# Kernel tuning notes

Hardware: AMD Instinct MI355X
Metric: run time of the kernel (lower is better)

The kernel has to match this reference:

```python
import jax, jax.numpy as jnp
import numpy as np

EPS = 1e-5

def layernorm(x, g, b):
    mu = jnp.mean(x, axis=-1, keepdims=True)
    var = jnp.mean(jnp.square(x - mu), axis=-1, keepdims=True)
    return (x - mu) * jax.lax.rsqrt(var + EPS) * g + b

def rope(x):
    # x: [B, H, S, hd]; faithful to source: theta = 10000**(-2*pos/hd), pos in {0,2,4,...}
    S, hd = x.shape[-2], x.shape[-1]
    pos2 = jnp.arange(0, hd, 2, dtype=jnp.float32)
    theta = jnp.power(10000.0, -2.0 * pos2 / hd)          # [hd/2]
    ang = jnp.arange(S, dtype=jnp.float32)[:, None] * theta  # [S, hd/2]
    cos, sin = jnp.cos(ang), jnp.sin(ang)                  # broadcast over B,H
    xr = x.reshape(*x.shape[:-1], hd // 2, 2)
    x0, x1 = xr[..., 0], xr[..., 1]
    out = jnp.stack([x0 * cos - x1 * sin, x1 * cos + x0 * sin], axis=-1)
    return out.reshape(x.shape)

def setup_inputs() -> dict:
    key = jax.random.key(0)
    ks = jax.random.split(key, 8)
    B, S, D, H = 2, 2048, 1024, 16
    hd = D // H
    s_in = 1.0 / np.sqrt(D)
    s_h = 1.0 / np.sqrt(2 * D)
    return {
        "x": jax.random.normal(ks[0], (B, S, D), jnp.float32),
        "ln1_g": jnp.ones((D,), jnp.float32),
        "ln1_b": jnp.zeros((D,), jnp.float32),
        "Wq": jax.random.normal(ks[1], (H, D, hd), jnp.float32) * s_in,
        "Wk": jax.random.normal(ks[2], (H, D, hd), jnp.float32) * s_in,
        "Wv": jax.random.normal(ks[3], (H, D, hd), jnp.float32) * s_in,
        "Wo": jax.random.normal(ks[4], (D, D), jnp.float32) * s_in,
        "ln2_g": jnp.ones((D,), jnp.float32),
        "ln2_b": jnp.zeros((D,), jnp.float32),
        "W1": jax.random.normal(ks[5], (D, 2 * D), jnp.float32) * s_in,
        "W2": jax.random.normal(ks[6], (D, 2 * D), jnp.float32) * s_in,
        "W3": jax.random.normal(ks[7], (2 * D, D), jnp.float32) * s_h,
    }

def reference(x, ln1_g, ln1_b, Wq, Wk, Wv, Wo, ln2_g, ln2_b, W1, W2, W3):
    B, S, D = x.shape
    # --- attention sublayer ---
    h = layernorm(x, ln1_g, ln1_b)
    q = jnp.einsum("bsd,hdk->bhsk", h, Wq)
    k = jnp.einsum("bsd,hdk->bhsk", h, Wk)
    v = jnp.einsum("bsd,hdk->bhsk", h, Wv)
    q, k = rope(q), rope(k)
    hd = q.shape[-1]
    scores = jnp.einsum("bhqk,bhsk->bhqs", q, k) * (hd ** -0.5)  # [B,H,S,S]
    causal = jnp.tril(jnp.ones((S, S), bool))
    scores = jnp.where(causal, scores, jnp.float32(-jnp.inf))
    attn = jax.nn.softmax(scores, axis=-1)
    o = jnp.einsum("bhqs,bhsk->bhqk", attn, v)                   # [B,H,S,hd]
    o = o.transpose(0, 2, 1, 3).reshape(B, S, D)                 # concat heads
    x = x + o @ Wo
    # --- SwiGLU FFN sublayer ---
    h2 = layernorm(x, ln2_g, ln2_b)
    u = h2 @ W1
    ffn = (u * jax.nn.sigmoid(u)) * (h2 @ W2)
    return x + ffn @ W3
```

## Files before the change

### kernel.cpp

```cpp
#include <hip/hip_runtime.h>
#include <hip/hip_bf16.h>

using bf16 = __hip_bfloat16;
typedef __attribute__((ext_vector_type(8))) short bf16x8;
typedef __attribute__((ext_vector_type(4))) float f32x4;


__device__ inline float toF(float x) { return x; }
__device__ inline float toF(bf16 x) { return __bfloat162float(x); }
__device__ inline void  stV(float* p, float v) { *p = v; }
__device__ inline void  stV(bf16* p, float v) { *p = __float2bfloat16(v); }

__device__ __forceinline__ void unpack8(uint4 u, float* f) {
    f[0] = __uint_as_float(u.x << 16); f[1] = __uint_as_float(u.x & 0xffff0000u);
    f[2] = __uint_as_float(u.y << 16); f[3] = __uint_as_float(u.y & 0xffff0000u);
    f[4] = __uint_as_float(u.z << 16); f[5] = __uint_as_float(u.z & 0xffff0000u);
    f[6] = __uint_as_float(u.w << 16); f[7] = __uint_as_float(u.w & 0xffff0000u);
}

__device__ __forceinline__ uint4 packbf8(const float* f) {
    union { unsigned short u[8]; uint4 v; } r;
#pragma unroll
    for (int i = 0; i < 8; i++) {
        bf16 b = __float2bfloat16(f[i]);
        r.u[i] = *(unsigned short*)&b;
    }
    return r.v;
}

__device__ __forceinline__ unsigned pack2(float lo, float hi) {
    bf16 a = __float2bfloat16(lo), b = __float2bfloat16(hi);
    return ((unsigned)*(unsigned short*)&b << 16) | (unsigned)*(unsigned short*)&a;
}

__device__ __forceinline__ void gl_lds16(const void* g, void* l) {
    __builtin_amdgcn_global_load_lds(
        (__attribute__((address_space(1))) void*)g,
        (__attribute__((address_space(3))) void*)l, 16, 0, 0);
}

template <typename Tx, typename To>
__global__ __launch_bounds__(256) void ln_kernel(
    const Tx* __restrict__ x, const float* __restrict__ g,
    const float* __restrict__ b, To* __restrict__ out)
{
    const int D = 1024;
    int row = blockIdx.x;
    int tid = threadIdx.x;
    const Tx* xr = x + (size_t)row * D;

    float vals[4];
    float sum = 0.f, sumsq = 0.f;
#pragma unroll
    for (int i = 0; i < 4; i++) {
        float v = toF(xr[tid + i * 256]);
        vals[i] = v; sum += v; sumsq += v * v;
    }
#pragma unroll
    for (int off = 32; off > 0; off >>= 1) {
        sum += __shfl_xor(sum, off);
        sumsq += __shfl_xor(sumsq, off);
    }
    __shared__ float s1[4], s2[4];
    int wave = tid >> 6, lane = tid & 63;
    if (lane == 0) { s1[wave] = sum; s2[wave] = sumsq; }
    __syncthreads();
    sum = s1[0] + s1[1] + s1[2] + s1[3];
    sumsq = s2[0] + s2[1] + s2[2] + s2[3];

    float mu = sum * (1.f / D);
    float var = sumsq * (1.f / D) - mu * mu;
    float rstd = rsqrtf(var + 1e-5f);

    To* orow = out + (size_t)row * D;
#pragma unroll
    for (int i = 0; i < 4; i++) {
        int c = tid + i * 256;
        stV(&orow[c], (vals[i] - mu) * rstd * g[c] + b[c]);
    }
}

__global__ __launch_bounds__(256) void tconv_kernel(
    const float* __restrict__ in, bf16* __restrict__ out, int R, int C)
{
    __shared__ float t[32][33];
    int hh = blockIdx.z;
    const float* ip = in + (size_t)hh * R * C;
    bf16* op = out + (size_t)hh * R * C;
    int c0 = blockIdx.x * 32, r0 = blockIdx.y * 32;
    int tx = threadIdx.x & 31, ty = threadIdx.x >> 5;
#pragma unroll
    for (int i = 0; i < 4; i++)
        t[ty + 8 * i][tx] = ip[(size_t)(r0 + ty + 8 * i) * C + c0 + tx];
    __syncthreads();
#pragma unroll
    for (int i = 0; i < 4; i++)
        op[(size_t)(c0 + ty + 8 * i) * R + r0 + tx] = __float2bfloat16(t[tx][ty + 8 * i]);
}

__global__ __launch_bounds__(256) void tconv3_kernel(
    const float* __restrict__ Aq, const float* __restrict__ Ak,
    const float* __restrict__ Av, bf16* __restrict__ out)
{
    __shared__ float t[32][33];
    int z = blockIdx.z;
    const float* in = (z < 16) ? Aq : (z < 32) ? Ak : Av;
    int hh = z & 15;
    const float* ip = in + (size_t)hh * 65536;
    bf16* op = out + ((size_t)(z >> 4) << 20) + (size_t)hh * 65536;
    int c0 = blockIdx.x * 32, r0 = blockIdx.y * 32;
    int tx = threadIdx.x & 31, ty = threadIdx.x >> 5;
#pragma unroll
    for (int i = 0; i < 4; i++)
        t[ty + 8 * i][tx] = ip[(size_t)(r0 + ty + 8 * i) * 64 + c0 + tx];
    __syncthreads();
#pragma unroll
    for (int i = 0; i < 4; i++)
        op[(size_t)(c0 + ty + 8 * i) * 1024 + r0 + tx] = __float2bfloat16(t[tx][ty + 8 * i]);
}

__global__ __launch_bounds__(256) void vtrans_kernel(
    const bf16* __restrict__ v, bf16* __restrict__ vt)
{
    __shared__ unsigned short t[64][68];
    int hh = blockIdx.y;
    int s0 = blockIdx.x * 64;
    int tid = threadIdx.x;
    int r = tid >> 2, g = (tid & 3) * 16;

    const uint4* src = (const uint4*)(v + ((size_t)hh * 2048 + s0 + r) * 64 + g);
    *(uint4*)&t[r][g] = src[0];
    *(uint4*)&t[r][g + 8] = src[1];
    __syncthreads();

    union { unsigned short u[16]; uint4 v4[2]; } o;
#pragma unroll
    for (int i = 0; i < 16; i++) o.u[i] = t[g + i][r];
    uint4* dst = (uint4*)(vt + ((size_t)hh * 64 + r) * 2048 + s0 + g);
    dst[0] = o.v4[0];
    dst[1] = o.v4[1];
}

template <int MODE>
__global__ __launch_bounds__(256) void mfma_gemm(
    const bf16* __restrict__ A, const bf16* __restrict__ BT0,
    void* __restrict__ Cv, const void* __restrict__ resv,
    int M, int N, int K)
{
    __shared__ bf16 smem[2][2][64 * 64];
    int tid = threadIdx.x, lane = tid & 63, w = tid >> 6;
    int wm = w >> 1, wn = w & 1;
    int m0 = blockIdx.y * 64, n0 = blockIdx.x * 64;

    const bf16* BT = BT0;
    bf16* Cq = nullptr; int rope = 0;
    if (MODE == 1) {
        int z = blockIdx.z;
        BT = BT0 + ((size_t)z << 20);
        Cq = (bf16*)Cv + ((size_t)z << 21);
        rope = (z < 2);
    }

    int lrow = lane >> 3;
    int lcb  = (lane & 7) ^ lrow;
    const bf16* Ag  = A  + (size_t)(m0 + w * 8 + lrow) * K + lcb * 8;
    const bf16* Bg0 = BT + (size_t)(n0 + w * 8 + lrow) * K + lcb * 8;
    unsigned sbase = (unsigned)__builtin_amdgcn_readfirstlane(w * 8 * 128);
    char* smc = (char*)smem;

    f32x4 acc[2][2], acc2[2][2];
#pragma unroll
    for (int i = 0; i < 2; i++)
#pragma unroll
        for (int j = 0; j < 2; j++) {
            acc[i][j] = (f32x4){0.f, 0.f, 0.f, 0.f};
            if (MODE == 5) acc2[i][j] = (f32x4){0.f, 0.f, 0.f, 0.f};
        }

    int cidx = lane & 15, quad = lane >> 4;

    auto run_pass = [&](const bf16* Bg, f32x4 (&ac)[2][2]) {
        auto STAGE = [&](int buf, int k0) {
            char* pA = smc + (size_t)buf * 16384 + sbase;
            char* pB = pA + 8192;
            gl_lds16(Ag + k0,                  pA);
            gl_lds16(Ag + (size_t)32 * K + k0, pA + 4096);
            gl_lds16(Bg + k0,                  pB);
            gl_lds16(Bg + (size_t)32 * K + k0, pB + 4096);
        };
        STAGE(0, 0);
        __syncthreads();
        int cur = 0;
        for (int k0 = 0; k0 < K; k0 += 64) {
            if (k0 + 64 < K) STAGE(cur ^ 1, k0 + 64);
            const bf16* Ab = (const bf16*)(smc + (size_t)cur * 16384);
            const bf16* Bb = Ab + 4096;
#pragma unroll
            for (int kk = 0; kk < 2; kk++) {
                int pb = (kk * 4 + quad) ^ (cidx & 7);
                bf16x8 af[2], bfr[2];
#pragma unroll
                for (int i = 0; i < 2; i++)
                    af[i] = *(const bf16x8*)&Ab[(wm * 32 + i * 16 + cidx) * 64 + pb * 8];
#pragma unroll
                for (int j = 0; j < 2; j++)
                    bfr[j] = *(const bf16x8*)&Bb[(wn * 32 + j * 16 + cidx) * 64 + pb * 8];
                __builtin_amdgcn_s_setprio(1);
#pragma unroll
                for (int i = 0; i < 2; i++)
#pragma unroll
                    for (int j = 0; j < 2; j++)
                        ac[i][j] = __builtin_amdgcn_mfma_f32_16x16x32_bf16(af[i], bfr[j], ac[i][j], 0, 0, 0);
                __builtin_amdgcn_s_setprio(0);
            }
            __syncthreads();
            cur ^= 1;
        }
    };

    run_pass(Bg0, acc);
    if (MODE == 5) {
        const bf16* B2g = (const bf16*)resv + (size_t)(n0 + w * 8 + lrow) * K + lcb * 8;
        run_pass(B2g, acc2);
    }

    int rbase = quad * 4;
#pragma unroll
    for (int i = 0; i < 2; i++) {
#pragma unroll
        for (int j = 0; j < 2; j++) {
#pragma unroll
            for (int r = 0; r < 4; r++) {
                int row = m0 + wm * 32 + i * 16 + rbase + r;
                int col = n0 + wn * 32 + j * 16 + cidx;
                float v = acc[i][j][r];
                size_t idx = (size_t)row * N + col;
                if (MODE == 1) {
                    int h = col >> 6, kk = col & 63;
                    float outv = v;
                    if (rope) {
                        float other = __shfl_xor(v, 1);
                        float p = (float)(kk >> 1);
                        float theta = __expf(p * -0.5756462732485114f);
                        float ang = (float)row * theta;
                        float c, sn; __sincosf(ang, &sn, &c);
                        outv = (kk & 1) ? (v * c + other * sn) : (v * c - other * sn);
                    }
                    Cq[((size_t)h * 2048 + row) * 64 + kk] = __float2bfloat16(outv);
                } else if (MODE == 2) {
                    v += ((const float*)resv)[idx];
                    ((bf16*)Cv)[idx] = __float2bfloat16(v);
                } else if (MODE == 5) {
                    float g2 = acc2[i][j][r];
                    float sg = 1.f / (1.f + __expf(-v));
                    ((bf16*)Cv)[idx] = __float2bfloat16(v * sg * g2);
                } else {
                    v += __bfloat162float(((const bf16*)resv)[idx]);
                    ((float*)Cv)[idx] = v;
                }
            }
        }
    }
}

__global__ __launch_bounds__(256) void attn_kernel(
    const bf16* __restrict__ q, const bf16* __restrict__ k,
    const bf16* __restrict__ vt, bf16* __restrict__ o)
{
    const int S = 2048;
    __shared__ bf16 Ks[64][72];
    __shared__ bf16 Vs[64][72];
    __shared__ __align__(16) char QPbuf[64 * 72 * 2];

    int h = blockIdx.y;
    int qt = (h & 8) ? (int)blockIdx.x : 31 - (int)blockIdx.x;
    int tid = threadIdx.x, lane = tid & 63, w = tid >> 6;
    int quad = lane >> 4, cidx = lane & 15;
    int m0 = qt * 64;

    const bf16* qb = q + ((size_t)h * S + m0) * 64;
    const bf16* kb = k + (size_t)h * S * 64;
    const bf16* vtb = vt + (size_t)h * 64 * S;

    int srow = tid >> 2;
    int sg = (tid & 3) * 16;

    bf16 (*Qs)[72] = (bf16 (*)[72])QPbuf;
    {
        const uint4* src = (const uint4*)(qb + (size_t)srow * 64 + sg);
        uint4 u0 = src[0], u1 = src[1];
        float f[16]; unpack8(u0, f); unpack8(u1, f + 8);
#pragma unroll
        for (int i = 0; i < 16; i++) f[i] *= 0.125f * 1.44269504f;
        *(uint4*)&Qs[srow][sg] = packbf8(f);
        *(uint4*)&Qs[srow][sg + 8] = packbf8(f + 8);
    }
    bf16x8 bQ0 = *(const bf16x8*)&Qs[w * 16 + cidx][quad * 8];
    bf16x8 bQ1 = *(const bf16x8*)&Qs[w * 16 + cidx][32 + quad * 8];

    unsigned* Pst = (unsigned*)QPbuf + w * 576;

    float m_i = -INFINITY, l_i = 0.f;
    f32x4 Oc[4];
#pragma unroll
    for (int i = 0; i < 4; i++) Oc[i] = (f32x4){0.f, 0.f, 0.f, 0.f};

    uint4 ka0, ka1, va0, va1;
    {
        const uint4* ksrc = (const uint4*)(kb + (size_t)srow * 64 + sg);
        ka0 = ksrc[0]; ka1 = ksrc[1];
        const uint4* vsrc = (const uint4*)(vtb + (size_t)srow * S + sg);
        va0 = vsrc[0]; va1 = vsrc[1];
    }

    for (int kt = 0; kt <= qt; kt++) {
        __syncthreads();
        *(uint4*)&Ks[srow][sg] = ka0; *(uint4*)&Ks[srow][sg + 8] = ka1;
        *(uint4*)&Vs[srow][sg] = va0; *(uint4*)&Vs[srow][sg + 8] = va1;
        __syncthreads();
        if (kt < qt) {
            const uint4* kn = (const uint4*)(kb + (size_t)((kt + 1) * 64 + srow) * 64 + sg);
            ka0 = kn[0]; ka1 = kn[1];
            const uint4* vn = (const uint4*)(vtb + (size_t)srow * S + (kt + 1) * 64 + sg);
            va0 = vn[0]; va1 = vn[1];
        }

        f32x4 sc[4];
#pragma unroll
        for (int i = 0; i < 4; i++) {
            bf16x8 aK0 = *(const bf16x8*)&Ks[i * 16 + cidx][quad * 8];
            bf16x8 aK1 = *(const bf16x8*)&Ks[i * 16 + cidx][32 + quad * 8];
            f32x4 z = (f32x4){0.f, 0.f, 0.f, 0.f};
            z = __builtin_amdgcn_mfma_f32_16x16x32_bf16(aK0, bQ0, z, 0, 0, 0);
            z = __builtin_amdgcn_mfma_f32_16x16x32_bf16(aK1, bQ1, z, 0, 0, 0);
            sc[i] = z;
        }

        if (kt == qt) {
#pragma unroll
            for (int i = 0; i < 4; i++)
#pragma unroll
                for (int r = 0; r < 4; r++)
                    if (i * 16 + quad * 4 + r > w * 16 + cidx) sc[i][r] = -INFINITY;
        }

        float pmax = sc[0][0];
#pragma unroll
        for (int i = 0; i < 4; i++)
#pragma unroll
            for (int r = 0; r < 4; r++) pmax = fmaxf(pmax, sc[i][r]);
        pmax = fmaxf(pmax, __shfl_xor(pmax, 16));
        pmax = fmaxf(pmax, __shfl_xor(pmax, 32));
        float mnew = fmaxf(m_i, pmax);
        float alpha = __builtin_amdgcn_exp2f(m_i - mnew);
        float rs = 0.f;
#pragma unroll
        for (int i = 0; i < 4; i++)
#pragma unroll
            for (int r = 0; r < 4; r++) {
                sc[i][r] = __builtin_amdgcn_exp2f(sc[i][r] - mnew);
                rs += sc[i][r];
            }
        rs += __shfl_xor(rs, 16);
        rs += __shfl_xor(rs, 32);
        l_i = l_i * alpha + rs;
        m_i = mnew;
#pragma unroll
        for (int i = 0; i < 4; i++) {
            Oc[i][0] *= alpha; Oc[i][1] *= alpha;
            Oc[i][2] *= alpha; Oc[i][3] *= alpha;
        }

#pragma unroll
        for (int i = 0; i < 4; i++) {
            uint2 t;
            t.x = pack2(sc[i][0], sc[i][1]);
            t.y = pack2(sc[i][2], sc[i][3]);
            *(uint2*)&Pst[cidx * 36 + 8 * i + 2 * quad] = t;
        }
        bf16x8 bP0 = *(const bf16x8*)&Pst[cidx * 36 + 4 * quad];
        bf16x8 bP1 = *(const bf16x8*)&Pst[cidx * 36 + 16 + 4 * quad];

#pragma unroll
        for (int i = 0; i < 4; i++) {
            bf16x8 aV0 = *(const bf16x8*)&Vs[i * 16 + cidx][quad * 8];
            bf16x8 aV1 = *(const bf16x8*)&Vs[i * 16 + cidx][32 + quad * 8];
            Oc[i] = __builtin_amdgcn_mfma_f32_16x16x32_bf16(aV0, bP0, Oc[i], 0, 0, 0);
            Oc[i] = __builtin_amdgcn_mfma_f32_16x16x32_bf16(aV1, bP1, Oc[i], 0, 0, 0);
        }
    }

    float inv = 1.f / l_i;
#pragma unroll
    for (int i = 0; i < 4; i++) {
        uint2 t;
        t.x = pack2(Oc[i][0] * inv, Oc[i][1] * inv);
        t.y = pack2(Oc[i][2] * inv, Oc[i][3] * inv);
        *(uint2*)&Pst[cidx * 36 + 8 * i + 2 * quad] = t;
    }
    int r2 = lane >> 2, g2 = (lane & 3) * 8;
    uint4 o0 = *(const uint4*)&Pst[r2 * 36 + g2];
    uint4 o1 = *(const uint4*)&Pst[r2 * 36 + g2 + 4];
    bf16* orow = o + (size_t)(m0 + w * 16 + r2) * 1024 + h * 64;
    *(uint4*)(orow + g2 * 2) = o0;
    *(uint4*)(orow + g2 * 2 + 8) = o1;
}

extern "C" void kernel_launch(void* const* d_in, const int* in_sizes, int n_in,
                              void* d_out, int out_size, void* d_ws, size_t ws_size,
                              hipStream_t stream)
{
    const int S = 2048, D = 1024;

    const float* x    = (const float*)d_in[0];
    const float* ln1g = (const float*)d_in[1];
    const float* ln1b = (const float*)d_in[2];
    const float* Wq   = (const float*)d_in[3];
    const float* Wk   = (const float*)d_in[4];
    const float* Wv   = (const float*)d_in[5];
    const float* Wo   = (const float*)d_in[6];
    const float* ln2g = (const float*)d_in[7];
    const float* ln2b = (const float*)d_in[8];
    const float* W1   = (const float*)d_in[9];
    const float* W2   = (const float*)d_in[10];
    const float* W3   = (const float*)d_in[11];
    float* out = (float*)d_out;

    const size_t NR = (size_t)S * D;
    bf16* r0 = (bf16*)d_ws;
    bf16* r1 = r0 + NR;
    bf16* r2 = r1 + NR;
    bf16* r3 = r2 + NR;
    const size_t M1 = 1u << 20;

    for (int b = 0; b < 2; b++) {
        const float* xb = x + (size_t)b * S * D;
        float* ob = out + (size_t)b * S * D;
        bf16* obB = (bf16*)ob;

        ln_kernel<float, bf16><<<S, 256, 0, stream>>>(xb, ln1g, ln1b, r3);

        tconv3_kernel<<<dim3(2, 32, 48), 256, 0, stream>>>(Wq, Wk, Wv, obB);

        mfma_gemm<1><<<dim3(16, 32, 3), 256, 0, stream>>>(r3, obB, r0, nullptr, S, 1024, 1024);

        vtrans_kernel<<<dim3(32, 16), 256, 0, stream>>>(r2, obB);

        attn_kernel<<<dim3(32, 16), 256, 0, stream>>>(r0, r1, obB, r2);

        tconv_kernel<<<dim3(32, 32, 1), 256, 0, stream>>>(Wo, obB + 2 * M1, 1024, 1024);
        mfma_gemm<2><<<dim3(16, 32, 1), 256, 0, stream>>>(r2, obB + 2 * M1, r3, xb, S, 1024, 1024);

        ln_kernel<bf16, bf16><<<S, 256, 0, stream>>>(r3, ln2g, ln2b, r0);

        tconv_kernel<<<dim3(64, 32, 1), 256, 0, stream>>>(W1, obB,          1024, 2048);
        tconv_kernel<<<dim3(64, 32, 1), 256, 0, stream>>>(W2, obB + 2 * M1, 1024, 2048);

        mfma_gemm<5><<<dim3(32, 32, 1), 256, 0, stream>>>(r0, obB, r1, obB + 2 * M1, S, 2048, 1024);

        tconv_kernel<<<dim3(32, 64, 1), 256, 0, stream>>>(W3, r0, 2048, 1024);

        mfma_gemm<4><<<dim3(16, 32, 1), 256, 0, stream>>>(r1, r0, ob, r3, S, 1024, 2048);
    }
}
```

Measured before the change: 382.2 us.

## Fuse weight transposes, write V pre-transposed, single-pass dual-B SwiGLU GEMM

New measurement: 368.9 us. 1.04x faster.

```diff
diff --git a/kernel.cpp b/kernel.cpp
--- a/kernel.cpp
+++ b/kernel.cpp
@@ -98,47 +98,49 @@
         op[(size_t)(c0 + ty + 8 * i) * R + r0 + tx] = __float2bfloat16(t[tx][ty + 8 * i]);
 }
 
-__global__ __launch_bounds__(256) void tconv3_kernel(
+__global__ __launch_bounds__(256) void tconv_w_kernel(
     const float* __restrict__ Aq, const float* __restrict__ Ak,
-    const float* __restrict__ Av, bf16* __restrict__ out)
+    const float* __restrict__ Av, const float* __restrict__ Ao,
+    bf16* __restrict__ out)
 {
     __shared__ float t[32][33];
     int z = blockIdx.z;
-    const float* in = (z < 16) ? Aq : (z < 32) ? Ak : Av;
-    int hh = z & 15;
-    const float* ip = in + (size_t)hh * 65536;
-    bf16* op = out + ((size_t)(z >> 4) << 20) + (size_t)hh * 65536;
+    const float* ip; int ldi;
+    if (z < 48) {
+        const float* s = (z < 16) ? Aq : (z < 32) ? Ak : Av;
+        ip = s + (size_t)(z & 15) * 65536; ldi = 64;
+    } else {
+        ip = Ao + (size_t)(z - 48) * 64; ldi = 1024;
+    }
+    bf16* op = out + ((size_t)z << 16);
     int c0 = blockIdx.x * 32, r0 = blockIdx.y * 32;
     int tx = threadIdx.x & 31, ty = threadIdx.x >> 5;
 #pragma unroll
     for (int i = 0; i < 4; i++)
-        t[ty + 8 * i][tx] = ip[(size_t)(r0 + ty + 8 * i) * 64 + c0 + tx];
+        t[ty + 8 * i][tx] = ip[(size_t)(r0 + ty + 8 * i) * ldi + c0 + tx];
     __syncthreads();
 #pragma unroll
     for (int i = 0; i < 4; i++)
         op[(size_t)(c0 + ty + 8 * i) * 1024 + r0 + tx] = __float2bfloat16(t[tx][ty + 8 * i]);
 }
 
-__global__ __launch_bounds__(256) void vtrans_kernel(
-    const bf16* __restrict__ v, bf16* __restrict__ vt)
-{
-    __shared__ unsigned short t[64][68];
-    int hh = blockIdx.y;
-    int s0 = blockIdx.x * 64;
-    int tid = threadIdx.x;
-    int r = tid >> 2, g = (tid & 3) * 16;
-
-    const uint4* src = (const uint4*)(v + ((size_t)hh * 2048 + s0 + r) * 64 + g);
-    *(uint4*)&t[r][g] = src[0];
-    *(uint4*)&t[r][g + 8] = src[1];
+__global__ __launch_bounds__(256) void tconv12_kernel(
+    const float* __restrict__ W1, const float* __restrict__ W2,
+    bf16* __restrict__ out)
+{
+    __shared__ float t[32][33];
+    int z = blockIdx.z;
+    const float* ip = z ? W2 : W1;
+    bf16* op = out + ((size_t)z << 21);
+    int c0 = blockIdx.x * 32, r0 = blockIdx.y * 32;
+    int tx = threadIdx.x & 31, ty = threadIdx.x >> 5;
+#pragma unroll
+    for (int i = 0; i < 4; i++)
+        t[ty + 8 * i][tx] = ip[(size_t)(r0 + ty + 8 * i) * 2048 + c0 + tx];
     __syncthreads();
-
-    union { unsigned short u[16]; uint4 v4[2]; } o;
-#pragma unroll
-    for (int i = 0; i < 16; i++) o.u[i] = t[g + i][r];
-    uint4* dst = (uint4*)(vt + ((size_t)hh * 64 + r) * 2048 + s0 + g);
-    dst[0] = o.v4[0];
-    dst[1] = o.v4[1];
+#pragma unroll
+    for (int i = 0; i < 4; i++)
+        op[(size_t)(c0 + ty + 8 * i) * 1024 + r0 + tx] = __float2bfloat16(t[tx][ty + 8 * i]);
 }
 
 template <int MODE>
@@ -147,7 +149,8 @@
     void* __restrict__ Cv, const void* __restrict__ resv,
     int M, int N, int K)
 {
-    __shared__ bf16 smem[2][2][64 * 64];
+    constexpr int NB = (MODE == 5) ? 3 : 2;
+    __shared__ bf16 smem[2][NB][64 * 64];
     int tid = threadIdx.x, lane = tid & 63, w = tid >> 6;
     int wm = w >> 1, wn = w & 1;
     int m0 = blockIdx.y * 64, n0 = blockIdx.x * 64;
@@ -165,6 +168,9 @@
     int lcb  = (lane & 7) ^ lrow;
     const bf16* Ag  = A  + (size_t)(m0 + w * 8 + lrow) * K + lcb * 8;
     const bf16* Bg0 = BT + (size_t)(n0 + w * 8 + lrow) * K + lcb * 8;
+    const bf16* B2g = (MODE == 5)
+        ? (const bf16*)resv + (size_t)(n0 + w * 8 + lrow) * K + lcb * 8
+        : nullptr;
     unsigned sbase = (unsigned)__builtin_amdgcn_readfirstlane(w * 8 * 128);
     char* smc = (char*)smem;
 
@@ -179,74 +185,85 @@
 
     int cidx = lane & 15, quad = lane >> 4;
 
-    auto run_pass = [&](const bf16* Bg, f32x4 (&ac)[2][2]) {
-        auto STAGE = [&](int buf, int k0) {
-            char* pA = smc + (size_t)buf * 16384 + sbase;
-            char* pB = pA + 8192;
-            gl_lds16(Ag + k0,                  pA);
-            gl_lds16(Ag + (size_t)32 * K + k0, pA + 4096);
-            gl_lds16(Bg + k0,                  pB);
-            gl_lds16(Bg + (size_t)32 * K + k0, pB + 4096);
-        };
-        STAGE(0, 0);
+    auto STAGE = [&](int buf, int k0) {
+        char* p = smc + (size_t)buf * (NB * 8192) + sbase;
+        gl_lds16(Ag + k0,                   p);
+        gl_lds16(Ag + (size_t)32 * K + k0,  p + 4096);
+        gl_lds16(Bg0 + k0,                  p + 8192);
+        gl_lds16(Bg0 + (size_t)32 * K + k0, p + 12288);
+        if (MODE == 5) {
+            gl_lds16(B2g + k0,                  p + 16384);
+            gl_lds16(B2g + (size_t)32 * K + k0, p + 20480);
+        }
+    };
+
+    STAGE(0, 0);
+    __syncthreads();
+    int cur = 0;
+    for (int k0 = 0; k0 < K; k0 += 64) {
+        if (k0 + 64 < K) STAGE(cur ^ 1, k0 + 64);
+        const bf16* Ab = (const bf16*)(smc + (size_t)cur * (NB * 8192));
+        const bf16* Bb = Ab + 4096;
+        const bf16* B2b = Ab + 8192;
+#pragma unroll
+        for (int kk = 0; kk < 2; kk++) {
+            int pb = (kk * 4 + quad) ^ (cidx & 7);
+            bf16x8 af[2], bfr[2], b2f[2];
+#pragma unroll
+            for (int i = 0; i < 2; i++)
+                af[i] = *(const bf16x8*)&Ab[(wm * 32 + i * 16 + cidx) * 64 + pb * 8];
+#pragma unroll
+            for (int j = 0; j < 2; j++)
+                bfr[j] = *(const bf16x8*)&Bb[(wn * 32 + j * 16 + cidx) * 64 + pb * 8];
+            if (MODE == 5) {
+#pragma unroll
+                for (int j = 0; j < 2; j++)
+                    b2f[j] = *(const bf16x8*)&B2b[(wn * 32 + j * 16 + cidx) * 64 + pb * 8];
+            }
+            __builtin_amdgcn_s_setprio(1);
+#pragma unroll
+            for (int i = 0; i < 2; i++)
+#pragma unroll
+                for (int j = 0; j < 2; j++) {
+                    acc[i][j] = __builtin_amdgcn_mfma_f32_16x16x32_bf16(af[i], bfr[j], acc[i][j], 0, 0, 0);
+                    if (MODE == 5)
+                        acc2[i][j] = __builtin_amdgcn_mfma_f32_16x16x32_bf16(af[i], b2f[j], acc2[i][j], 0, 0, 0);
+                }
+            __builtin_amdgcn_s_setprio(0);
+        }
         __syncthreads();
-        int cur = 0;
-        for (int k0 = 0; k0 < K; k0 += 64) {
-            if (k0 + 64 < K) STAGE(cur ^ 1, k0 + 64);
-            const bf16* Ab = (const bf16*)(smc + (size_t)cur * 16384);
-            const bf16* Bb = Ab + 4096;
-#pragma unroll
-            for (int kk = 0; kk < 2; kk++) {
-                int pb = (kk * 4 + quad) ^ (cidx & 7);
-                bf16x8 af[2], bfr[2];
-#pragma unroll
-                for (int i = 0; i < 2; i++)
-                    af[i] = *(const bf16x8*)&Ab[(wm * 32 + i * 16 + cidx) * 64 + pb * 8];
-#pragma unroll
-                for (int j = 0; j < 2; j++)
-                    bfr[j] = *(const bf16x8*)&Bb[(wn * 32 + j * 16 + cidx) * 64 + pb * 8];
-                __builtin_amdgcn_s_setprio(1);
-#pragma unroll
-                for (int i = 0; i < 2; i++)
-#pragma unroll
-                    for (int j = 0; j < 2; j++)
-                        ac[i][j] = __builtin_amdgcn_mfma_f32_16x16x32_bf16(af[i], bfr[j], ac[i][j], 0, 0, 0);
-                __builtin_amdgcn_s_setprio(0);
+        cur ^= 1;
+    }
+
+    int rbase = quad * 4;
+#pragma unroll
+    for (int i = 0; i < 2; i++) {
+#pragma unroll
+        for (int j = 0; j < 2; j++) {
+            int row0 = m0 + wm * 32 + i * 16 + rbase;
+            int col = n0 + wn * 32 + j * 16 + cidx;
+            if (MODE == 1 && !rope) {
+                int h_ = col >> 6, d = col & 63;
+                uint2 t;
+                t.x = pack2(acc[i][j][0], acc[i][j][1]);
+                t.y = pack2(acc[i][j][2], acc[i][j][3]);
+                *(uint2*)&Cq[(size_t)h_ * 131072 + (size_t)d * 2048 + row0] = t;
+                continue;
             }
-            __syncthreads();
-            cur ^= 1;
-        }
-    };
-
-    run_pass(Bg0, acc);
-    if (MODE == 5) {
-        const bf16* B2g = (const bf16*)resv + (size_t)(n0 + w * 8 + lrow) * K + lcb * 8;
-        run_pass(B2g, acc2);
-    }
-
-    int rbase = quad * 4;
-#pragma unroll
-    for (int i = 0; i < 2; i++) {
-#pragma unroll
-        for (int j = 0; j < 2; j++) {
 #pragma unroll
             for (int r = 0; r < 4; r++) {
-                int row = m0 + wm * 32 + i * 16 + rbase + r;
-                int col = n0 + wn * 32 + j * 16 + cidx;
+                int row = row0 + r;
                 float v = acc[i][j][r];
                 size_t idx = (size_t)row * N + col;
                 if (MODE == 1) {
-                    int h = col >> 6, kk = col & 63;
-                    float outv = v;
-                    if (rope) {
-                        float other = __shfl_xor(v, 1);
-                        float p = (float)(kk >> 1);
-                        float theta = __expf(p * -0.5756462732485114f);
-                        float ang = (float)row * theta;
-                        float c, sn; __sincosf(ang, &sn, &c);
-                        outv = (kk & 1) ? (v * c + other * sn) : (v * c - other * sn);
-                    }
-                    Cq[((size_t)h * 2048 + row) * 64 + kk] = __float2bfloat16(outv);
+                    int h_ = col >> 6, kk = col & 63;
+                    float other = __shfl_xor(v, 1);
+                    float p = (float)(kk >> 1);
+                    float theta = __expf(p * -0.5756462732485114f);
+                    float ang = (float)row * theta;
+                    float c, sn; __sincosf(ang, &sn, &c);
+                    float outv = (kk & 1) ? (v * c + other * sn) : (v * c - other * sn);
+                    Cq[((size_t)h_ * 2048 + row) * 64 + kk] = __float2bfloat16(outv);
                 } else if (MODE == 2) {
                     v += ((const float*)resv)[idx];
                     ((bf16*)Cv)[idx] = __float2bfloat16(v);
@@ -436,27 +453,23 @@
     for (int b = 0; b < 2; b++) {
         const float* xb = x + (size_t)b * S * D;
         float* ob = out + (size_t)b * S * D;
-        bf16* obB = (bf16*)ob;
+        bf16* pb = (bf16*)ob;
 
         ln_kernel<float, bf16><<<S, 256, 0, stream>>>(xb, ln1g, ln1b, r3);
 
-        tconv3_kernel<<<dim3(2, 32, 48), 256, 0, stream>>>(Wq, Wk, Wv, obB);
-
-        mfma_gemm<1><<<dim3(16, 32, 3), 256, 0, stream>>>(r3, obB, r0, nullptr, S, 1024, 1024);
-
-        vtrans_kernel<<<dim3(32, 16), 256, 0, stream>>>(r2, obB);
-
-        attn_kernel<<<dim3(32, 16), 256, 0, stream>>>(r0, r1, obB, r2);
-
-        tconv_kernel<<<dim3(32, 32, 1), 256, 0, stream>>>(Wo, obB + 2 * M1, 1024, 1024);
-        mfma_gemm<2><<<dim3(16, 32, 1), 256, 0, stream>>>(r2, obB + 2 * M1, r3, xb, S, 1024, 1024);
+        tconv_w_kernel<<<dim3(2, 32, 64), 256, 0, stream>>>(Wq, Wk, Wv, Wo, pb);
+
+        mfma_gemm<1><<<dim3(16, 32, 3), 256, 0, stream>>>(r3, pb, r0, nullptr, S, 1024, 1024);
+
+        attn_kernel<<<dim3(32, 16), 256, 0, stream>>>(r0, r1, r2, pb);
+
+        mfma_gemm<2><<<dim3(16, 32, 1), 256, 0, stream>>>(pb, pb + 3 * M1, r3, xb, S, 1024, 1024);
 
         ln_kernel<bf16, bf16><<<S, 256, 0, stream>>>(r3, ln2g, ln2b, r0);
 
-        tconv_kernel<<<dim3(64, 32, 1), 256, 0, stream>>>(W1, obB,          1024, 2048);
-        tconv_kernel<<<dim3(64, 32, 1), 256, 0, stream>>>(W2, obB + 2 * M1, 1024, 2048);
-
-        mfma_gemm<5><<<dim3(32, 32, 1), 256, 0, stream>>>(r0, obB, r1, obB + 2 * M1, S, 2048, 1024);
+        tconv12_kernel<<<dim3(64, 32, 2), 256, 0, stream>>>(W1, W2, pb);
+
+        mfma_gemm<5><<<dim3(32, 32, 1), 256, 0, stream>>>(r0, pb, r1, pb + 2 * M1, S, 2048, 1024);
 
         tconv_kernel<<<dim3(32, 64, 1), 256, 0, stream>>>(W3, r0, 2048, 1024);
 
```
